# Kernel tuning notes

Measured on AMD Instinct MI355X. Metric: run time of the kernel, lower is better.

The kernel has to match this reference:

```python
import jax, jax.numpy as jnp
import numpy as np

OUT_FEATURES = 512
IN_FEATURES = 512


def _unfold_tt(G1, G2):
    # G1: (1, do0, r, di0), G2: (r, do1, 1, di1)
    # einsum 'abcd,cefg->abefdg' then reshape -> (out_features, in_features)
    W = jnp.einsum('abcd,cefg->abefdg', G1, G2)
    return W.reshape(OUT_FEATURES, IN_FEATURES)


def setup_inputs() -> dict:
    key = jax.random.key(0)
    ks = jax.random.split(key, 5)
    std = np.sqrt(2.0 / IN_FEATURES).astype(np.float32)
    x = jax.random.normal(ks[0], (8, 4096, 2 * IN_FEATURES), dtype=jnp.float32)
    G1_R = jax.random.uniform(ks[1], (1, 32, 4, 32), jnp.float32, -std, std)
    G2_R = jax.random.uniform(ks[2], (4, 16, 1, 16), jnp.float32, -std, std)
    G1_I = jax.random.uniform(ks[3], (1, 32, 4, 32), jnp.float32, -std, std)
    G2_I = jax.random.uniform(ks[4], (4, 16, 1, 16), jnp.float32, -std, std)
    bias_real = jnp.zeros((OUT_FEATURES,), jnp.float32)
    bias_imag = jnp.zeros((OUT_FEATURES,), jnp.float32)
    return {"x": x, "G1_R": G1_R, "G2_R": G2_R, "G1_I": G1_I, "G2_I": G2_I,
            "bias_real": bias_real, "bias_imag": bias_imag}


def reference(x, G1_R, G2_R, G1_I, G2_I, bias_real, bias_imag):
    W_real = _unfold_tt(G1_R, G2_R)  # (out, in)
    W_imag = _unfold_tt(G1_I, G2_I)
    x_real, x_imag = jnp.split(x, 2, axis=-1)
    # F.linear(x, W, b) = x @ W.T + b
    out_real = x_real @ W_real.T - x_imag @ W_imag.T + bias_real
    out_imag = x_real @ W_imag.T + x_imag @ W_real.T + bias_imag
    return jnp.concatenate([out_real, out_imag], axis=-1)
```

## Files before the change

### kernel.cpp

```cpp
#include <hip/hip_runtime.h>
#include <hip/hip_bf16.h>
#include <stdint.h>


typedef _Float16 half8 __attribute__((ext_vector_type(8)));
typedef _Float16 half4v __attribute__((ext_vector_type(4)));
typedef float f32x4 __attribute__((ext_vector_type(4)));

typedef __attribute__((address_space(3))) void* lds_ptr_t;
typedef const __attribute__((address_space(1))) void* gbl_ptr_t;

__device__ __forceinline__ void gload_lds16(const void* g, void* s) {
  __builtin_amdgcn_global_load_lds((gbl_ptr_t)g, (lds_ptr_t)s, 16, 0, 0);
}

__global__ void build_bt(const float* __restrict__ G1R, const float* __restrict__ G2R,
                         const float* __restrict__ G1I, const float* __restrict__ G2I,
                         _Float16* __restrict__ BT) {
  int idx = blockIdx.x * 256 + threadIdx.x;
  int n = idx >> 10, k = idx & 1023;
  int o = n & 511, i = k & 511;
  bool imagOut = n >= 512, kHi = k >= 512;
  const float* G1;
  const float* G2;
  float sign = 1.0f;
  if (imagOut == kHi) { G1 = G1R; G2 = G2R; }
  else { G1 = G1I; G2 = G2I; if (!imagOut) sign = -1.0f; }
  int b = o >> 4, e = o & 15, d = i >> 4, g = i & 15;
  float w = 0.0f;
#pragma unroll
  for (int c = 0; c < 4; ++c)
    w += G1[b * 128 + c * 32 + d] * G2[c * 256 + e * 16 + g];
  BT[idx] = (_Float16)(sign * w);
}

__global__ __launch_bounds__(256, 2) void tt_gemm(
    const float* __restrict__ A,
    const _Float16* __restrict__ BT,
    const float* __restrict__ bias_r, const float* __restrict__ bias_i,
    float* __restrict__ C) {
  __shared__ __align__(16) _Float16 Als[128 * 32];
  __shared__ __align__(16) _Float16 Bls[128 * 32];

  const int tid = threadIdx.x;
  const int bid = blockIdx.x;
  const int bid2 = (bid & 7) * 256 + (bid >> 3);
  const int mt = bid2 >> 3, nt = bid2 & 7;
  const int row0 = mt * 128, col0 = nt * 128;

  const int lane = tid & 63, wid = tid >> 6;
  const int wm = wid >> 1, wn = wid & 1;
  const int lr = lane & 15, lq = lane >> 4;

  f32x4 acc[4][4] = {};

  const int brow_base = wid * 32 + (lane >> 2);
  const int bk = (lane & 3) * 8;

  const float* Abase = A + (size_t)row0 * 1024;

  for (int kt = 0; kt < 32; ++kt) {
    const int k0 = kt * 32;
    float4 va[4];
#pragma unroll
    for (int i = 0; i < 4; ++i) {
      int fid = i * 256 + tid;
      int ar = fid >> 3, aq = fid & 7;
      va[i] = *(const float4*)(Abase + (size_t)ar * 1024 + k0 + aq * 4);
    }
    __syncthreads();
#pragma unroll
    for (int i = 0; i < 4; ++i) {
      int fid = i * 256 + tid;
      int ar = fid >> 3, aq = fid & 7;
      half4v h = { (_Float16)va[i].x, (_Float16)va[i].y,
                   (_Float16)va[i].z, (_Float16)va[i].w };
      *(half4v*)&Als[ar * 32 + aq * 4] = h;
    }
#pragma unroll
    for (int j = 0; j < 2; ++j) {
      gload_lds16(BT + (size_t)(col0 + brow_base + j * 16) * 1024 + k0 + bk,
                  (char*)Bls + (wid * 2 + j) * 1024);
    }
    __syncthreads();
    half8 af[4], bf[4];
#pragma unroll
    for (int m = 0; m < 4; ++m)
      af[m] = *(const half8*)&Als[(wm * 64 + m * 16 + lr) * 32 + lq * 8];
#pragma unroll
    for (int n = 0; n < 4; ++n)
      bf[n] = *(const half8*)&Bls[(wn * 64 + n * 16 + lr) * 32 + lq * 8];
#pragma unroll
    for (int m = 0; m < 4; ++m)
#pragma unroll
      for (int n = 0; n < 4; ++n)
        acc[m][n] = __builtin_amdgcn_mfma_f32_16x16x32_f16(af[m], bf[n], acc[m][n], 0, 0, 0);
  }

#pragma unroll
  for (int n = 0; n < 4; ++n) {
    int col = col0 + wn * 64 + n * 16 + lr;
    float bias = (col < 512) ? bias_r[col] : bias_i[col - 512];
#pragma unroll
    for (int m = 0; m < 4; ++m) {
      int r0 = row0 + wm * 64 + m * 16 + lq * 4;
#pragma unroll
      for (int r = 0; r < 4; ++r)
        C[(size_t)(r0 + r) * 1024 + col] = acc[m][n][r] + bias;
    }
  }
}

extern "C" void kernel_launch(void* const* d_in, const int* in_sizes, int n_in,
                              void* d_out, int out_size, void* d_ws, size_t ws_size,
                              hipStream_t stream) {
  const float* x   = (const float*)d_in[0];
  const float* G1R = (const float*)d_in[1];
  const float* G2R = (const float*)d_in[2];
  const float* G1I = (const float*)d_in[3];
  const float* G2I = (const float*)d_in[4];
  const float* br  = (const float*)d_in[5];
  const float* bi  = (const float*)d_in[6];
  float* out = (float*)d_out;
  _Float16* BT = (_Float16*)d_ws;

  build_bt<<<4096, 256, 0, stream>>>(G1R, G2R, G1I, G2I, BT);
  tt_gemm<<<2048, 256, 0, stream>>>(x, BT, br, bi, out);
}
```

Before: 116.9 us.

## Pre-pack A and B into MFMA fragment layout and drop LDS staging

Adds a separate pass that converts x to fp16 and stores it in per-lane MFMA fragment order. B is stored in the same fragment-major order. The GEMM then loads fragments straight from global memory into registers, with no LDS or barriers, and prefetches the next k-step while it computes. Each wave now owns a 128x64 tile with 8x4 accumulators, and s_setprio is raised around the MFMA bursts. The cost is an extra full pass that reads x and writes a half-size copy, plus heavier register pressure and reliance on L2 to reuse fragments across waves.

```diff
diff --git a/kernel.cpp b/kernel.cpp
--- a/kernel.cpp
+++ b/kernel.cpp
@@ -4,109 +4,132 @@
 
 
 typedef _Float16 half8 __attribute__((ext_vector_type(8)));
-typedef _Float16 half4v __attribute__((ext_vector_type(4)));
 typedef float f32x4 __attribute__((ext_vector_type(4)));
 
-typedef __attribute__((address_space(3))) void* lds_ptr_t;
-typedef const __attribute__((address_space(1))) void* gbl_ptr_t;
-
-__device__ __forceinline__ void gload_lds16(const void* g, void* s) {
-  __builtin_amdgcn_global_load_lds((gbl_ptr_t)g, (lds_ptr_t)s, 16, 0, 0);
-}
+#define PRIO1() __builtin_amdgcn_s_setprio(1)
+#define PRIO0() __builtin_amdgcn_s_setprio(0)
 
 __global__ void build_bt(const float* __restrict__ G1R, const float* __restrict__ G2R,
                          const float* __restrict__ G1I, const float* __restrict__ G2I,
                          _Float16* __restrict__ BT) {
   int idx = blockIdx.x * 256 + threadIdx.x;
-  int n = idx >> 10, k = idx & 1023;
+  int e    = idx & 7;
+  int lane = (idx >> 3) & 63;
+  int kk   = (idx >> 9) & 1;
+  int j    = (idx >> 10) & 3;
+  int t    = (idx >> 12) & 15;
+  int ng   = idx >> 16;
+  int n = ng * 64 + j * 16 + (lane & 15);
+  int k = t * 64 + kk * 32 + (lane >> 4) * 8 + e;
   int o = n & 511, i = k & 511;
   bool imagOut = n >= 512, kHi = k >= 512;
-  const float* G1;
-  const float* G2;
-  float sign = 1.0f;
+  const float* G1; const float* G2; float sign = 1.0f;
   if (imagOut == kHi) { G1 = G1R; G2 = G2R; }
   else { G1 = G1I; G2 = G2I; if (!imagOut) sign = -1.0f; }
-  int b = o >> 4, e = o & 15, d = i >> 4, g = i & 15;
+  int b = o >> 4, ee = o & 15, d = i >> 4, g = i & 15;
   float w = 0.0f;
 #pragma unroll
   for (int c = 0; c < 4; ++c)
-    w += G1[b * 128 + c * 32 + d] * G2[c * 256 + e * 16 + g];
+    w += G1[b * 128 + c * 32 + d] * G2[c * 256 + ee * 16 + g];
   BT[idx] = (_Float16)(sign * w);
 }
 
+__global__ __launch_bounds__(256) void build_at(const float* __restrict__ X,
+                                                _Float16* __restrict__ Aimg) {
+  int ci = blockIdx.x * 256 + threadIdx.x;
+  int lane = ci & 63;
+  int kk   = (ci >> 6) & 1;
+  int t    = (ci >> 7) & 15;
+  int g16  = ci >> 11;
+  int row = g16 * 16 + (lane & 15);
+  int k0  = t * 64 + kk * 32 + (lane >> 4) * 8;
+  const float* s = X + (size_t)row * 1024 + k0;
+  float4 v0 = *(const float4*)s;
+  float4 v1 = *(const float4*)(s + 4);
+  half8 h = { (_Float16)v0.x, (_Float16)v0.y, (_Float16)v0.z, (_Float16)v0.w,
+              (_Float16)v1.x, (_Float16)v1.y, (_Float16)v1.z, (_Float16)v1.w };
+  *(half8*)((char*)Aimg + (size_t)ci * 16) = h;
+}
+
 __global__ __launch_bounds__(256, 2) void tt_gemm(
-    const float* __restrict__ A,
-    const _Float16* __restrict__ BT,
+    const _Float16* __restrict__ Aimg, const _Float16* __restrict__ Bimg,
     const float* __restrict__ bias_r, const float* __restrict__ bias_i,
     float* __restrict__ C) {
-  __shared__ __align__(16) _Float16 Als[128 * 32];
-  __shared__ __align__(16) _Float16 Bls[128 * 32];
+  const int tid = threadIdx.x, bid = blockIdx.x;
+  const int w = tid >> 6, lane = tid & 63;
+  const int lr = lane & 15, lq = lane >> 4;
+  const int lb = bid >> 3;
+  const int ng  = (bid & 7) * 2 + (lb >> 6);
+  const int mtb = lb & 63;
+  const int g16b = (mtb * 4 + w) * 8;
 
-  const int tid = threadIdx.x;
-  const int bid = blockIdx.x;
-  const int bid2 = (bid & 7) * 256 + (bid >> 3);
-  const int mt = bid2 >> 3, nt = bid2 & 7;
-  const int row0 = mt * 128, col0 = nt * 128;
+  const char* Ab = (const char*)Aimg + (size_t)lane * 16;
+  const char* Bb = (const char*)Bimg + (size_t)lane * 16;
 
-  const int lane = tid & 63, wid = tid >> 6;
-  const int wm = wid >> 1, wn = wid & 1;
-  const int lr = lane & 15, lq = lane >> 4;
+  f32x4 acc[8][4] = {};
+  half8 afr[8][2], bfr[4][2];
 
-  f32x4 acc[4][4] = {};
+  auto aaddr = [&](int mf, int t, int kk) {
+    return (const half8*)(Ab + ((size_t)(((g16b + mf) * 16 + t) * 2 + kk) << 10));
+  };
+  auto baddr = [&](int j, int t, int kk) {
+    return (const half8*)(Bb + ((size_t)((ng * 16 + t) * 8 + j * 2 + kk) << 10));
+  };
 
-  const int brow_base = wid * 32 + (lane >> 2);
-  const int bk = (lane & 3) * 8;
-
-  const float* Abase = A + (size_t)row0 * 1024;
-
-  for (int kt = 0; kt < 32; ++kt) {
-    const int k0 = kt * 32;
-    float4 va[4];
 #pragma unroll
-    for (int i = 0; i < 4; ++i) {
-      int fid = i * 256 + tid;
-      int ar = fid >> 3, aq = fid & 7;
-      va[i] = *(const float4*)(Abase + (size_t)ar * 1024 + k0 + aq * 4);
-    }
-    __syncthreads();
+  for (int mf = 0; mf < 8; ++mf) {
+    afr[mf][0] = *aaddr(mf, 0, 0);
+    afr[mf][1] = *aaddr(mf, 0, 1);
+  }
 #pragma unroll
-    for (int i = 0; i < 4; ++i) {
-      int fid = i * 256 + tid;
-      int ar = fid >> 3, aq = fid & 7;
-      half4v h = { (_Float16)va[i].x, (_Float16)va[i].y,
-                   (_Float16)va[i].z, (_Float16)va[i].w };
-      *(half4v*)&Als[ar * 32 + aq * 4] = h;
-    }
-#pragma unroll
-    for (int j = 0; j < 2; ++j) {
-      gload_lds16(BT + (size_t)(col0 + brow_base + j * 16) * 1024 + k0 + bk,
-                  (char*)Bls + (wid * 2 + j) * 1024);
-    }
-    __syncthreads();
-    half8 af[4], bf[4];
-#pragma unroll
-    for (int m = 0; m < 4; ++m)
-      af[m] = *(const half8*)&Als[(wm * 64 + m * 16 + lr) * 32 + lq * 8];
-#pragma unroll
-    for (int n = 0; n < 4; ++n)
-      bf[n] = *(const half8*)&Bls[(wn * 64 + n * 16 + lr) * 32 + lq * 8];
-#pragma unroll
-    for (int m = 0; m < 4; ++m)
-#pragma unroll
-      for (int n = 0; n < 4; ++n)
-        acc[m][n] = __builtin_amdgcn_mfma_f32_16x16x32_f16(af[m], bf[n], acc[m][n], 0, 0, 0);
+  for (int j = 0; j < 4; ++j) {
+    bfr[j][0] = *baddr(j, 0, 0);
+    bfr[j][1] = *baddr(j, 0, 1);
   }
 
+  for (int t = 0; t < 16; ++t) {
+    PRIO1();
 #pragma unroll
-  for (int n = 0; n < 4; ++n) {
-    int col = col0 + wn * 64 + n * 16 + lr;
+    for (int mf = 0; mf < 8; ++mf)
+#pragma unroll
+      for (int j = 0; j < 4; ++j)
+        acc[mf][j] = __builtin_amdgcn_mfma_f32_16x16x32_f16(
+            afr[mf][0], bfr[j][0], acc[mf][j], 0, 0, 0);
+    PRIO0();
+    if (t < 15) {
+#pragma unroll
+      for (int mf = 0; mf < 8; ++mf) afr[mf][0] = *aaddr(mf, t + 1, 0);
+#pragma unroll
+      for (int j = 0; j < 4; ++j)    bfr[j][0] = *baddr(j, t + 1, 0);
+    }
+    PRIO1();
+#pragma unroll
+    for (int mf = 0; mf < 8; ++mf)
+#pragma unroll
+      for (int j = 0; j < 4; ++j)
+        acc[mf][j] = __builtin_amdgcn_mfma_f32_16x16x32_f16(
+            afr[mf][1], bfr[j][1], acc[mf][j], 0, 0, 0);
+    PRIO0();
+    if (t < 15) {
+#pragma unroll
+      for (int mf = 0; mf < 8; ++mf) afr[mf][1] = *aaddr(mf, t + 1, 1);
+#pragma unroll
+      for (int j = 0; j < 4; ++j)    bfr[j][1] = *baddr(j, t + 1, 1);
+    }
+  }
+
+  const int row0 = (mtb * 4 + w) * 128;
+  const int col0 = ng * 64;
+#pragma unroll
+  for (int j = 0; j < 4; ++j) {
+    int col = col0 + j * 16 + lr;
     float bias = (col < 512) ? bias_r[col] : bias_i[col - 512];
 #pragma unroll
-    for (int m = 0; m < 4; ++m) {
-      int r0 = row0 + wm * 64 + m * 16 + lq * 4;
+    for (int mf = 0; mf < 8; ++mf) {
+      int r0 = row0 + mf * 16 + lq * 4;
 #pragma unroll
       for (int r = 0; r < 4; ++r)
-        C[(size_t)(r0 + r) * 1024 + col] = acc[m][n][r] + bias;
+        C[(size_t)(r0 + r) * 1024 + col] = acc[mf][j][r] + bias;
     }
   }
 }
@@ -122,8 +145,11 @@
   const float* br  = (const float*)d_in[5];
   const float* bi  = (const float*)d_in[6];
   float* out = (float*)d_out;
-  _Float16* BT = (_Float16*)d_ws;
 
-  build_bt<<<4096, 256, 0, stream>>>(G1R, G2R, G1I, G2I, BT);
-  tt_gemm<<<2048, 256, 0, stream>>>(x, BT, br, bi, out);
+  _Float16* Bimg = (_Float16*)d_ws;
+  _Float16* Aimg = (_Float16*)((char*)d_ws + (2u << 20));
+
+  build_bt<<<4096, 256, 0, stream>>>(G1R, G2R, G1I, G2I, Bimg);
+  build_at<<<16384, 256, 0, stream>>>(x, Aimg);
+  tt_gemm<<<1024, 256, 0, stream>>>(Aimg, Bimg, br, bi, out);
 }
```

After: 220.4 us. +88.5%, slower.
